# Kernel tuning notes

Measured on AMD Instinct MI355X. Metric: run time of the kernel, lower is better.

## Reference

```python
import jax, jax.numpy as jnp
import numpy as np

VOCAB = 50000   # vocab.count
EMBED = 256     # args.embed
B = 16          # batch
C = 64          # uniform context_len per example (stack() requires it)
S = 512         # src_seq == qry_seq == args.max_in_seq
UNK = 1         # vocab.w2i['<UNK>']


def setup_inputs() -> dict:
    key = jax.random.key(0)
    k1, k2, k3, k4 = jax.random.split(key, 4)
    sources = jax.random.randint(k1, (B * C, S), 0, VOCAB)
    # queries: contiguous nonzero prefix of length q_len in [S//2, S], zeros after
    ids = jax.random.randint(k2, (B, S), 1, VOCAB)
    qlens = jax.random.randint(k3, (B,), S // 2, S + 1)
    queries = jnp.where(jnp.arange(S)[None, :] < qlens[:, None], ids, 0)
    emb = jax.random.normal(k4, (VOCAB, EMBED), dtype=jnp.float32)
    return {"sources": sources, "queries": queries, "context_len": C, "emb": emb}


def reference(sources, queries, context_len, emb):
    vocab = emb.shape[0]
    # unk_tensor: clamp out-of-vocab ids to <UNK>
    src_ids = jnp.where(sources >= vocab, UNK, sources)
    q_ids = jnp.where(queries >= vocab, UNK, queries)
    b, s = queries.shape
    # [b, C, S, D] embedded sources; [b, S, D] embedded queries
    es = emb[src_ids].reshape(b, context_len, s, emb.shape[1])
    eq = emb[q_ids]
    # q_len slicing == masking since nonzero query prefix is contiguous
    qmask = (queries > 0).astype(emb.dtype)            # [b, S]
    # score[b,c] = sum_{j < q_len_b} <es[b,c,j], eq[b,j]>
    scores = jnp.einsum('bcsd,bsd->bc', es, eq * qmask[:, :, None])
    sims = jax.nn.softmax(scores, axis=1)              # per-example softmax over context
    top = jnp.argmax(scores, axis=1)                   # argmax of sim == argmax of scores
    src3 = sources.reshape(b, context_len, s)
    out_sources = jnp.take_along_axis(src3, top[:, None, None], axis=1).squeeze(1)
    return out_sources, sims
```

## Files before the change

kernel.cpp:

```cpp
#include <hip/hip_runtime.h>

#define VOCAB 50000
#define EMBED 256
#define NB    16
#define NC    64
#define NS    512
#define UNK   1

#define CTILE 8
#define JT    8
#define JLEN  (NS / JT)

__global__ __launch_bounds__(256) void scores_kernel(
    const int* __restrict__ src, const int* __restrict__ q,
    const float* __restrict__ emb, float* __restrict__ partial)
{
    const int x  = blockIdx.x;
    const int jt = x & (JT - 1);
    const int ct = (x >> 3) & (NC / CTILE - 1);
    const int b  = x >> 6;
    const int c0 = ct * CTILE;
    const int j0 = jt * JLEN;

    const int tid  = threadIdx.x;
    const int wave = tid >> 6;
    const int lane = tid & 63;

    const float4* __restrict__ emb4 = (const float4*)emb;
    const int* __restrict__ qrow = q + (size_t)b * NS;
    const int* __restrict__ srow = src + ((size_t)b * NC + c0) * NS;

    float acc[CTILE];
#pragma unroll
    for (int i = 0; i < CTILE; i++) acc[i] = 0.f;

    for (int j = j0 + wave; j < j0 + JLEN; j += 4) {
        const int qv = qrow[j];
        if (qv > 0) {
            const int qid = (qv >= VOCAB) ? UNK : qv;
            const float4 eq = emb4[(size_t)qid * (EMBED / 4) + lane];

            int sid[CTILE];
#pragma unroll
            for (int i = 0; i < CTILE; i++) {
                const int sv = srow[(size_t)i * NS + j];
                sid[i] = (sv >= VOCAB) ? UNK : sv;
            }
            float4 a[CTILE];
#pragma unroll
            for (int i = 0; i < CTILE; i++)
                a[i] = emb4[(size_t)sid[i] * (EMBED / 4) + lane];
#pragma unroll
            for (int i = 0; i < CTILE; i++)
                acc[i] += a[i].x * eq.x + a[i].y * eq.y + a[i].z * eq.z + a[i].w * eq.w;
        }
    }

#pragma unroll
    for (int off = 32; off > 0; off >>= 1)
#pragma unroll
        for (int i = 0; i < CTILE; i++)
            acc[i] += __shfl_down(acc[i], off, 64);

    __shared__ float red[4][CTILE];
    if (lane == 0)
#pragma unroll
        for (int i = 0; i < CTILE; i++) red[wave][i] = acc[i];
    __syncthreads();

    if (tid < CTILE) {
        const float s = red[0][tid] + red[1][tid] + red[2][tid] + red[3][tid];
        partial[(size_t)jt * (NB * NC) + b * NC + c0 + tid] = s;
    }
}

__global__ __launch_bounds__(256) void finalize_kernel(
    const float* __restrict__ partial, const int* __restrict__ src,
    float* __restrict__ out)
{
    const int b   = blockIdx.x;
    const int tid = threadIdx.x;

    __shared__ int top_sh;

    if (tid < 64) {
        const int c = tid;
        float s = 0.f;
#pragma unroll
        for (int jt = 0; jt < JT; jt++)
            s += partial[(size_t)jt * (NB * NC) + b * NC + c];

        float m = s;
#pragma unroll
        for (int off = 32; off > 0; off >>= 1)
            m = fmaxf(m, __shfl_xor(m, off, 64));

        const float e = expf(s - m);
        float sum = e;
#pragma unroll
        for (int off = 32; off > 0; off >>= 1)
            sum += __shfl_xor(sum, off, 64);

        out[NB * NS + b * NC + c] = e / sum;

        const unsigned long long ballot = __ballot(s == m);
        if (tid == 0) top_sh = __ffsll(ballot) - 1;
    }
    __syncthreads();

    const int top = top_sh;
    const int* __restrict__ srow = src + ((size_t)b * NC + top) * NS;
#pragma unroll
    for (int j = tid; j < NS; j += 256)
        out[b * NS + j] = (float)srow[j];
}

extern "C" void kernel_launch(void* const* d_in, const int* in_sizes, int n_in,
                              void* d_out, int out_size, void* d_ws, size_t ws_size,
                              hipStream_t stream) {
    const int*   src = (const int*)d_in[0];
    const int*   q   = (const int*)d_in[1];
    const float* emb = (const float*)d_in[3];

    float* out     = (float*)d_out;
    float* partial = (float*)d_ws;

    scores_kernel<<<NB * (NC / CTILE) * JT, 256, 0, stream>>>(src, q, emb, partial);
    finalize_kernel<<<NB, 256, 0, stream>>>(partial, src, out);
}
```

Baseline: 150.8 us.

## Fuse finalize into scores kernel via last-block atomic counter, double j-split

The separate finalize kernel is removed. The last scores block to finish, detected through an atomic counter in workspace, now computes the softmax, the argmax and the gather of the winning source row for all batches. The j dimension is split into 16 tiles instead of 8, which doubles the block count to raise parallelism. The change adds a memset launch and a serialized tail run by a single block, and it depends on threadfence ordering to be correct.

New measurement: 210.3 us. +39.5%, slower.

```diff
diff --git a/kernel.cpp b/kernel.cpp
--- a/kernel.cpp
+++ b/kernel.cpp
@@ -8,17 +8,19 @@
 #define UNK   1
 
 #define CTILE 8
-#define JT    8
+#define JT    16
 #define JLEN  (NS / JT)
+#define NBLOCKS (NB * (NC / CTILE) * JT)
 
 __global__ __launch_bounds__(256) void scores_kernel(
     const int* __restrict__ src, const int* __restrict__ q,
-    const float* __restrict__ emb, float* __restrict__ partial)
+    const float* __restrict__ emb, float* __restrict__ partial,
+    unsigned int* __restrict__ done, float* __restrict__ out)
 {
     const int x  = blockIdx.x;
     const int jt = x & (JT - 1);
-    const int ct = (x >> 3) & (NC / CTILE - 1);
-    const int b  = x >> 6;
+    const int ct = (x >> 4) & (NC / CTILE - 1);
+    const int b  = x >> 7;
     const int c0 = ct * CTILE;
     const int j0 = jt * JLEN;
 
@@ -72,23 +74,26 @@
         const float s = red[0][tid] + red[1][tid] + red[2][tid] + red[3][tid];
         partial[(size_t)jt * (NB * NC) + b * NC + c0 + tid] = s;
     }
-}
 
-__global__ __launch_bounds__(256) void finalize_kernel(
-    const float* __restrict__ partial, const int* __restrict__ src,
-    float* __restrict__ out)
-{
-    const int b   = blockIdx.x;
-    const int tid = threadIdx.x;
+    __shared__ int is_last;
+    __syncthreads();
+    if (tid == 0) {
+        __threadfence();
+        is_last = (atomicAdd(done, 1u) == NBLOCKS - 1u) ? 1 : 0;
+    }
+    __syncthreads();
+    if (!is_last) return;
+    __threadfence();
 
-    __shared__ int top_sh;
+    const int w = wave;
+#pragma unroll
+    for (int bi = 0; bi < 4; bi++) {
+        const int bb = w * 4 + bi;
 
-    if (tid < 64) {
-        const int c = tid;
         float s = 0.f;
 #pragma unroll
-        for (int jt = 0; jt < JT; jt++)
-            s += partial[(size_t)jt * (NB * NC) + b * NC + c];
+        for (int t = 0; t < JT; t++)
+            s += partial[(size_t)t * (NB * NC) + bb * NC + lane];
 
         float m = s;
 #pragma unroll
@@ -101,18 +106,16 @@
         for (int off = 32; off > 0; off >>= 1)
             sum += __shfl_xor(sum, off, 64);
 
-        out[NB * NS + b * NC + c] = e / sum;
+        out[NB * NS + bb * NC + lane] = e / sum;
 
         const unsigned long long ballot = __ballot(s == m);
-        if (tid == 0) top_sh = __ffsll(ballot) - 1;
+        const int top = __ffsll(ballot) - 1;
+
+        const int* __restrict__ trow = src + ((size_t)bb * NC + top) * NS;
+#pragma unroll
+        for (int j = lane; j < NS; j += 64)
+            out[bb * NS + j] = (float)trow[j];
     }
-    __syncthreads();
-
-    const int top = top_sh;
-    const int* __restrict__ srow = src + ((size_t)b * NC + top) * NS;
-#pragma unroll
-    for (int j = tid; j < NS; j += 256)
-        out[b * NS + j] = (float)srow[j];
 }
 
 extern "C" void kernel_launch(void* const* d_in, const int* in_sizes, int n_in,
@@ -124,7 +127,8 @@
 
     float* out     = (float*)d_out;
     float* partial = (float*)d_ws;
+    unsigned int* done = (unsigned int*)((char*)d_ws + (size_t)JT * NB * NC * sizeof(float));
 
-    scores_kernel<<<NB * (NC / CTILE) * JT, 256, 0, stream>>>(src, q, emb, partial);
-    finalize_kernel<<<NB, 256, 0, stream>>>(partial, src, out);
+    hipMemsetAsync(done, 0, sizeof(unsigned int), stream);
+    scores_kernel<<<NBLOCKS, 256, 0, stream>>>(src, q, emb, partial, done, out);
 }
```

## Gather source embeddings from a bf16 copy of the table, stage queries in LDS

Applied to the files above, without the earlier changes.

Each call adds a kernel that converts the fp32 embedding table to bf16 in workspace. The scores kernel then gathers source rows at half the bytes, caches the fp32 query embeddings and clamped source ids in shared memory, and loops only over the nonzero query prefix. The j-split doubles to 16 tiles for more blocks. The conversion reads the full 51 MB table every call, which may cost more than the gather bandwidth it saves. bf16 rounding of source embeddings also risks score and argmax mismatches. A fallback fp32 path is kept for when workspace is too small.

Measured after the change: 132.8 us. 1.14x faster.

```diff
diff --git a/kernel.cpp b/kernel.cpp
--- a/kernel.cpp
+++ b/kernel.cpp
@@ -8,17 +8,41 @@
 #define UNK   1
 
 #define CTILE 8
-#define JT    8
+#define JT    16
 #define JLEN  (NS / JT)
-
-__global__ __launch_bounds__(256) void scores_kernel(
+#define BF_TABLE_BYTES ((size_t)VOCAB * EMBED * 2)
+#define PARTIAL_ELEMS  (JT * NB * NC)
+
+__device__ __forceinline__ unsigned short f2bf_rne(float f) {
+    unsigned int u = __float_as_uint(f);
+    u = (u + 0x7fffu + ((u >> 16) & 1u)) >> 16;
+    return (unsigned short)u;
+}
+
+__global__ __launch_bounds__(256) void convert_kernel(
+    const float* __restrict__ emb, unsigned int* __restrict__ bf)
+{
+    const size_t t = (size_t)blockIdx.x * 256 + threadIdx.x;
+    const float4* __restrict__ e4 = (const float4*)emb;
+    const float4 a = e4[t * 2];
+    const float4 b = e4[t * 2 + 1];
+    uint4 r;
+    r.x = (unsigned int)f2bf_rne(a.x) | ((unsigned int)f2bf_rne(a.y) << 16);
+    r.y = (unsigned int)f2bf_rne(a.z) | ((unsigned int)f2bf_rne(a.w) << 16);
+    r.z = (unsigned int)f2bf_rne(b.x) | ((unsigned int)f2bf_rne(b.y) << 16);
+    r.w = (unsigned int)f2bf_rne(b.z) | ((unsigned int)f2bf_rne(b.w) << 16);
+    ((uint4*)bf)[t] = r;
+}
+
+__global__ __launch_bounds__(256) void scores_bf_kernel(
     const int* __restrict__ src, const int* __restrict__ q,
-    const float* __restrict__ emb, float* __restrict__ partial)
+    const float* __restrict__ emb, const unsigned int* __restrict__ bf,
+    float* __restrict__ partial)
 {
     const int x  = blockIdx.x;
     const int jt = x & (JT - 1);
-    const int ct = (x >> 3) & (NC / CTILE - 1);
-    const int b  = x >> 6;
+    const int ct = (x >> 4) & (NC / CTILE - 1);
+    const int b  = x >> 7;
     const int c0 = ct * CTILE;
     const int j0 = jt * JLEN;
 
@@ -27,35 +51,110 @@
     const int lane = tid & 63;
 
     const float4* __restrict__ emb4 = (const float4*)emb;
+    const uint2*  __restrict__ bfe  = (const uint2*)bf;
     const int* __restrict__ qrow = q + (size_t)b * NS;
     const int* __restrict__ srow = src + ((size_t)b * NC + c0) * NS;
 
+    __shared__ float qt[JLEN][EMBED];
+    __shared__ int   sids[CTILE][JLEN];
+    __shared__ int   qids[JLEN];
+    __shared__ int   nnz_sh;
+
+    if (tid < 64) {
+        const int qv = (tid < JLEN) ? qrow[j0 + tid] : 0;
+        if (tid < JLEN) qids[tid] = (qv >= VOCAB) ? UNK : qv;
+        const unsigned long long bal = __ballot(qv > 0);
+        if (tid == 0) nnz_sh = __popcll(bal);
+    }
+    {
+        const int i = tid >> 5, j = tid & 31;
+        const int sv = srow[(size_t)i * NS + j0 + j];
+        sids[i][j] = (sv >= VOCAB) ? UNK : sv;
+    }
+    __syncthreads();
+
+    const int nnz = nnz_sh;
+
+    float4* qt4 = (float4*)qt;
+    for (int r = wave; r < nnz; r += 4)
+        qt4[r * 64 + lane] = emb4[(size_t)qids[r] * (EMBED / 4) + lane];
+    __syncthreads();
+
     float acc[CTILE];
 #pragma unroll
     for (int i = 0; i < CTILE; i++) acc[i] = 0.f;
 
-    for (int j = j0 + wave; j < j0 + JLEN; j += 4) {
+#pragma unroll 2
+    for (int j = wave; j < nnz; j += 4) {
+        const float4 qv = qt4[j * 64 + lane];
+        uint2 a[CTILE];
+#pragma unroll
+        for (int i = 0; i < CTILE; i++)
+            a[i] = bfe[(size_t)sids[i][j] * 64 + lane];
+#pragma unroll
+        for (int i = 0; i < CTILE; i++) {
+            const float f0 = __uint_as_float(a[i].x << 16);
+            const float f1 = __uint_as_float(a[i].x & 0xffff0000u);
+            const float f2 = __uint_as_float(a[i].y << 16);
+            const float f3 = __uint_as_float(a[i].y & 0xffff0000u);
+            acc[i] += f0 * qv.x + f1 * qv.y + f2 * qv.z + f3 * qv.w;
+        }
+    }
+
+#pragma unroll
+    for (int off = 32; off > 0; off >>= 1)
+#pragma unroll
+        for (int i = 0; i < CTILE; i++)
+            acc[i] += __shfl_down(acc[i], off, 64);
+
+    __shared__ float red[4][CTILE];
+    if (lane == 0)
+#pragma unroll
+        for (int i = 0; i < CTILE; i++) red[wave][i] = acc[i];
+    __syncthreads();
+
+    if (tid < CTILE) {
+        const float s = red[0][tid] + red[1][tid] + red[2][tid] + red[3][tid];
+        partial[(size_t)jt * (NB * NC) + b * NC + c0 + tid] = s;
+    }
+}
+
+__global__ __launch_bounds__(256) void scores_f32_kernel(
+    const int* __restrict__ src, const int* __restrict__ q,
+    const float* __restrict__ emb, float* __restrict__ partial)
+{
+    const int x  = blockIdx.x;
+    const int jt = x & 7;
+    const int ct = (x >> 3) & 7;
+    const int b  = x >> 6;
+    const int c0 = ct * CTILE;
+    const int j0 = jt * 64;
+
+    const int tid = threadIdx.x, wave = tid >> 6, lane = tid & 63;
+    const float4* __restrict__ emb4 = (const float4*)emb;
+    const int* __restrict__ qrow = q + (size_t)b * NS;
+    const int* __restrict__ srow = src + ((size_t)b * NC + c0) * NS;
+
+    float acc[CTILE];
+#pragma unroll
+    for (int i = 0; i < CTILE; i++) acc[i] = 0.f;
+
+    for (int j = j0 + wave; j < j0 + 64; j += 4) {
         const int qv = qrow[j];
         if (qv > 0) {
             const int qid = (qv >= VOCAB) ? UNK : qv;
             const float4 eq = emb4[(size_t)qid * (EMBED / 4) + lane];
-
-            int sid[CTILE];
+            float4 a[CTILE];
 #pragma unroll
             for (int i = 0; i < CTILE; i++) {
                 const int sv = srow[(size_t)i * NS + j];
-                sid[i] = (sv >= VOCAB) ? UNK : sv;
+                a[i] = emb4[(size_t)((sv >= VOCAB) ? UNK : sv) * (EMBED / 4) + lane];
             }
-            float4 a[CTILE];
-#pragma unroll
-            for (int i = 0; i < CTILE; i++)
-                a[i] = emb4[(size_t)sid[i] * (EMBED / 4) + lane];
 #pragma unroll
             for (int i = 0; i < CTILE; i++)
                 acc[i] += a[i].x * eq.x + a[i].y * eq.y + a[i].z * eq.z + a[i].w * eq.w;
         }
     }
-
 #pragma unroll
     for (int off = 32; off > 0; off >>= 1)
 #pragma unroll
@@ -67,41 +166,34 @@
 #pragma unroll
         for (int i = 0; i < CTILE; i++) red[wave][i] = acc[i];
     __syncthreads();
-
-    if (tid < CTILE) {
-        const float s = red[0][tid] + red[1][tid] + red[2][tid] + red[3][tid];
-        partial[(size_t)jt * (NB * NC) + b * NC + c0 + tid] = s;
-    }
+    if (tid < CTILE)
+        partial[(size_t)jt * (NB * NC) + b * NC + c0 + tid] =
+            red[0][tid] + red[1][tid] + red[2][tid] + red[3][tid];
 }
 
 __global__ __launch_bounds__(256) void finalize_kernel(
     const float* __restrict__ partial, const int* __restrict__ src,
-    float* __restrict__ out)
-{
-    const int b   = blockIdx.x;
-    const int tid = threadIdx.x;
-
+    float* __restrict__ out, int jtn)
+{
+    const int b = blockIdx.x, tid = threadIdx.x;
     __shared__ int top_sh;
 
     if (tid < 64) {
-        const int c = tid;
         float s = 0.f;
-#pragma unroll
-        for (int jt = 0; jt < JT; jt++)
-            s += partial[(size_t)jt * (NB * NC) + b * NC + c];
+        for (int t = 0; t < jtn; t++)
+            s += partial[(size_t)t * (NB * NC) + b * NC + tid];
 
         float m = s;
 #pragma unroll
         for (int off = 32; off > 0; off >>= 1)
             m = fmaxf(m, __shfl_xor(m, off, 64));
-
         const float e = expf(s - m);
         float sum = e;
 #pragma unroll
         for (int off = 32; off > 0; off >>= 1)
             sum += __shfl_xor(sum, off, 64);
 
-        out[NB * NS + b * NC + c] = e / sum;
+        out[NB * NS + b * NC + tid] = e / sum;
 
         const unsigned long long ballot = __ballot(s == m);
         if (tid == 0) top_sh = __ffsll(ballot) - 1;
@@ -110,7 +202,6 @@
 
     const int top = top_sh;
     const int* __restrict__ srow = src + ((size_t)b * NC + top) * NS;
-#pragma unroll
     for (int j = tid; j < NS; j += 256)
         out[b * NS + j] = (float)srow[j];
 }
@@ -121,10 +212,17 @@
     const int*   src = (const int*)d_in[0];
     const int*   q   = (const int*)d_in[1];
     const float* emb = (const float*)d_in[3];
-
-    float* out     = (float*)d_out;
-    float* partial = (float*)d_ws;
-
-    scores_kernel<<<NB * (NC / CTILE) * JT, 256, 0, stream>>>(src, q, emb, partial);
-    finalize_kernel<<<NB, 256, 0, stream>>>(partial, src, out);
-}
+    float* out = (float*)d_out;
+
+    if (ws_size >= BF_TABLE_BYTES + PARTIAL_ELEMS * sizeof(float)) {
+        unsigned int* bf = (unsigned int*)d_ws;
+        float* partial = (float*)((char*)d_ws + BF_TABLE_BYTES);
+        convert_kernel<<<VOCAB * EMBED / 2048, 256, 0, stream>>>(emb, bf);
+        scores_bf_kernel<<<NB * (NC / CTILE) * JT, 256, 0, stream>>>(src, q, emb, bf, partial);
+        finalize_kernel<<<NB, 256, 0, stream>>>(partial, src, out, JT);
+    } else {
+        float* partial = (float*)d_ws;
+        scores_f32_kernel<<<NB * 8 * 8, 256, 0, stream>>>(src, q, emb, partial);
+        finalize_kernel<<<NB, 256, 0, stream>>>(partial, src, out, 8);
+    }
+}
```
